# Optimization experiments

Hardware: AMD Instinct MI355X
Metric: run time of the kernel (lower is better)

Reference implementation:

```python
import jax, jax.numpy as jnp
import numpy as np

TEMPERATURE = 8.0
EPS = 1e-8  # torch F.cosine_similarity clamps each norm at eps=1e-8

B, L, H, D = 4, 1024, 8, 64


def setup_inputs() -> dict:
    key = jax.random.key(0)
    kq, kk, kv = jax.random.split(key, 3)
    q = jax.random.normal(kq, (B, L, H, D), dtype=jnp.float32)
    k = jax.random.normal(kk, (B, L, H, D), dtype=jnp.float32)
    v = jax.random.normal(kv, (B, L, H, D), dtype=jnp.float32)
    return {"q": q, "k": k, "v": v}


def _l2_normalize(x):
    # matches torch cosine_similarity: divide by max(||x||, eps)
    n = jnp.sqrt(jnp.sum(x * x, axis=-1, keepdims=True))
    return x / jnp.maximum(n, EPS)


def reference(q, k, v):
    # [B, L, H, D] -> [B, H, L, D]
    qt = jnp.swapaxes(q, 1, 2)
    kt = jnp.swapaxes(k, 1, 2)
    vt = jnpp = jnp.swapaxes(v, 1, 2)
    qn = _l2_normalize(qt)
    kn = _l2_normalize(kt)
    # cosine similarity via matmul instead of O(L*L*D) broadcast
    attn = jnp.einsum("bhid,bhjd->bhij", qn, kn) / TEMPERATURE  # [B,H,L,L]
    attn = jax.nn.softmax(attn, axis=-1)
    out = jnp.einsum("bhij,bhjd->bhid", attn, vt)  # [B,H,L,D]
    return out, attn
```

## Files before the change

### kernel.cpp

```cpp
#include <hip/hip_runtime.h>

#define NB 4
#define NL 1024
#define NH 8
#define ND 64
#define NBH 32

typedef __attribute__((ext_vector_type(8))) short bhalf8;
typedef __attribute__((ext_vector_type(4))) float f32x4;

static __device__ inline unsigned short f2bf(float f) {
    union { float f; unsigned u; } x; x.f = f;
    unsigned r = x.u + 0x7FFFu + ((x.u >> 16) & 1u);
    return (unsigned short)(r >> 16);
}

__global__ __launch_bounds__(256) void norm_qk_kernel(const float* __restrict__ q,
                                                      const float* __restrict__ k,
                                                      unsigned short* __restrict__ qn,
                                                      unsigned short* __restrict__ kn) {
    int wid  = threadIdx.x >> 6;
    int lane = threadIdx.x & 63;
    int r = blockIdx.x * 4 + wid;
    int b = r >> 13;
    int l = (r >> 3) & (NL - 1);
    int h = r & (NH - 1);

    float qv = q[(size_t)r * ND + lane];
    float kv = k[(size_t)r * ND + lane];
    float qs = qv * qv, ks = kv * kv;
    #pragma unroll
    for (int m = 1; m < 64; m <<= 1) {
        qs += __shfl_xor(qs, m);
        ks += __shfl_xor(ks, m);
    }
    float qd = 1.0f / (fmaxf(sqrtf(qs), 1e-8f) * 8.0f);
    float kd = 1.0f / fmaxf(sqrtf(ks), 1e-8f);

    size_t o = ((size_t)(b * NH + h) * NL + l) * ND + lane;
    qn[o] = f2bf(qv * qd);
    kn[o] = f2bf(kv * kd);
}

__global__ __launch_bounds__(256) void vtrans_kernel(const float* __restrict__ v,
                                                     unsigned short* __restrict__ vt) {
    __shared__ float tile[64 * 65];
    int bh = blockIdx.x;
    int b = bh >> 3, h = bh & 7;
    int l0 = blockIdx.y * 64;
    int wid = threadIdx.x >> 6, lane = threadIdx.x & 63;

    #pragma unroll
    for (int rr = 0; rr < 16; ++rr) {
        int row = rr * 4 + wid;
        float val = v[(((size_t)b * NL + l0 + row) * NH + h) * ND + lane];
        tile[lane * 65 + row] = val;
    }
    __syncthreads();
    #pragma unroll
    for (int dd = 0; dd < 16; ++dd) {
        int d = dd * 4 + wid;
        vt[((size_t)(bh * ND + d)) * NL + l0 + lane] = f2bf(tile[d * 65 + lane]);
    }
}

__global__ __launch_bounds__(256) void attn_kernel(const unsigned short* __restrict__ qn,
                                                   const unsigned short* __restrict__ kn,
                                                   const unsigned short* __restrict__ vt,
                                                   float* __restrict__ outp,
                                                   float* __restrict__ attnp) {
    int bh   = blockIdx.x;
    int wid  = threadIdx.x >> 6;
    int lane = threadIdx.x & 63;
    int c    = lane & 15;
    int quad = lane >> 4;
    int qt   = blockIdx.y * 4 + wid;
    int m0   = qt * 16;

    __shared__ __align__(16) unsigned short ptile[4][16 * 40];
    unsigned short* myp = &ptile[wid][0];

    const unsigned short* qbase = qn + ((size_t)(bh * NL + m0 + c)) * ND + quad * 8;
    bhalf8 qa0 = *(const bhalf8*)(qbase);
    bhalf8 qa1 = *(const bhalf8*)(qbase + 32);

    const unsigned short* kbh = kn + (size_t)bh * NL * ND;

    float denom[4] = {0.f, 0.f, 0.f, 0.f};
    for (int jt = 0; jt < 64; ++jt) {
        const unsigned short* kb = kbh + ((size_t)(jt * 16 + c)) * ND + quad * 8;
        bhalf8 kf0 = *(const bhalf8*)(kb);
        bhalf8 kf1 = *(const bhalf8*)(kb + 32);
        f32x4 s = {0.f, 0.f, 0.f, 0.f};
        s = __builtin_amdgcn_mfma_f32_16x16x32_bf16(qa0, kf0, s, 0, 0, 0);
        s = __builtin_amdgcn_mfma_f32_16x16x32_bf16(qa1, kf1, s, 0, 0, 0);
        #pragma unroll
        for (int r = 0; r < 4; ++r) denom[r] += __expf(s[r]);
    }
    #pragma unroll
    for (int r = 0; r < 4; ++r) {
        float d = denom[r];
        d += __shfl_xor(d, 1);
        d += __shfl_xor(d, 2);
        d += __shfl_xor(d, 4);
        d += __shfl_xor(d, 8);
        denom[r] = 1.0f / d;
    }

    float* attnrow = attnp + ((size_t)(bh * NL + m0)) * NL;
    const unsigned short* vbh = vt + (size_t)bh * ND * NL;

    f32x4 o[4] = {{0.f,0.f,0.f,0.f},{0.f,0.f,0.f,0.f},{0.f,0.f,0.f,0.f},{0.f,0.f,0.f,0.f}};
    for (int j2 = 0; j2 < 32; ++j2) {
        int jb = j2 * 32;
        #pragma unroll
        for (int sub = 0; sub < 2; ++sub) {
            int j0 = jb + sub * 16;
            const unsigned short* kb = kbh + ((size_t)(j0 + c)) * ND + quad * 8;
            bhalf8 kf0 = *(const bhalf8*)(kb);
            bhalf8 kf1 = *(const bhalf8*)(kb + 32);
            f32x4 s = {0.f, 0.f, 0.f, 0.f};
            s = __builtin_amdgcn_mfma_f32_16x16x32_bf16(qa0, kf0, s, 0, 0, 0);
            s = __builtin_amdgcn_mfma_f32_16x16x32_bf16(qa1, kf1, s, 0, 0, 0);
            #pragma unroll
            for (int r = 0; r < 4; ++r) {
                float a = __expf(s[r]) * denom[r];
                attnrow[(size_t)(quad * 4 + r) * NL + j0 + c] = a;
                myp[(quad * 4 + r) * 40 + sub * 16 + c] = f2bf(a);
            }
        }
        bhalf8 pa = *(const bhalf8*)(myp + c * 40 + quad * 8);
        #pragma unroll
        for (int nt = 0; nt < 4; ++nt) {
            const unsigned short* vb = vbh + (size_t)(nt * 16 + c) * NL + jb + quad * 8;
            bhalf8 vf = *(const bhalf8*)(vb);
            o[nt] = __builtin_amdgcn_mfma_f32_16x16x32_bf16(pa, vf, o[nt], 0, 0, 0);
        }
    }

    float* obase = outp + ((size_t)(bh * NL + m0)) * ND;
    #pragma unroll
    for (int nt = 0; nt < 4; ++nt) {
        #pragma unroll
        for (int r = 0; r < 4; ++r) {
            obase[(size_t)(quad * 4 + r) * ND + nt * 16 + c] = o[nt][r];
        }
    }
}

extern "C" void kernel_launch(void* const* d_in, const int* in_sizes, int n_in,
                              void* d_out, int out_size, void* d_ws, size_t ws_size,
                              hipStream_t stream) {
    const float* q = (const float*)d_in[0];
    const float* k = (const float*)d_in[1];
    const float* v = (const float*)d_in[2];

    float* outp  = (float*)d_out;
    float* attnp = outp + (size_t)NB * NH * NL * ND;

    unsigned short* qn = (unsigned short*)d_ws;
    unsigned short* kn = qn + (size_t)NB * NH * NL * ND;
    unsigned short* vt = kn + (size_t)NB * NH * NL * ND;

    norm_qk_kernel<<<(NB * NL * NH) / 4, 256, 0, stream>>>(q, k, qn, kn);
    vtrans_kernel<<<dim3(NBH, NL / 64), 256, 0, stream>>>(v, vt);
    attn_kernel<<<dim3(NBH, NL / 16 / 4), 256, 0, stream>>>(qn, kn, vt, outp, attnp);
}
```

Measured before the change: 235.0 us.

## Split key dimension across waves in attention and use exp2 with folded scale

The attention kernel now gives each block one 16-row query tile and splits the 1024 keys across its four waves. Each wave computes a partial softmax denominator and a partial output, and both are combined through shared memory with block barriers. This creates four times as many blocks and shortens each wave's serial key loop. The temperature scaling is folded with log2(e) into the query normalization so the kernel can call the hardware exp2 directly. The V transpose kernel moves to 1024-thread blocks. In exchange, Q fragments are loaded more times and the kernel adds barriers plus a shared-memory reduction.

```diff
diff --git a/kernel.cpp b/kernel.cpp
--- a/kernel.cpp
+++ b/kernel.cpp
@@ -34,7 +34,7 @@
         qs += __shfl_xor(qs, m);
         ks += __shfl_xor(ks, m);
     }
-    float qd = 1.0f / (fmaxf(sqrtf(qs), 1e-8f) * 8.0f);
+    float qd = 1.0f / (fmaxf(sqrtf(qs), 1e-8f) * 5.545177444479562f);
     float kd = 1.0f / fmaxf(sqrtf(ks), 1e-8f);
 
     size_t o = ((size_t)(b * NH + h) * NL + l) * ND + lane;
@@ -42,8 +42,8 @@
     kn[o] = f2bf(kv * kd);
 }
 
-__global__ __launch_bounds__(256) void vtrans_kernel(const float* __restrict__ v,
-                                                     unsigned short* __restrict__ vt) {
+__global__ __launch_bounds__(1024) void vtrans_kernel(const float* __restrict__ v,
+                                                      unsigned short* __restrict__ vt) {
     __shared__ float tile[64 * 65];
     int bh = blockIdx.x;
     int b = bh >> 3, h = bh & 7;
@@ -51,15 +51,15 @@
     int wid = threadIdx.x >> 6, lane = threadIdx.x & 63;
 
     #pragma unroll
-    for (int rr = 0; rr < 16; ++rr) {
-        int row = rr * 4 + wid;
+    for (int rr = 0; rr < 4; ++rr) {
+        int row = wid * 4 + rr;
         float val = v[(((size_t)b * NL + l0 + row) * NH + h) * ND + lane];
         tile[lane * 65 + row] = val;
     }
     __syncthreads();
     #pragma unroll
-    for (int dd = 0; dd < 16; ++dd) {
-        int d = dd * 4 + wid;
+    for (int dd = 0; dd < 4; ++dd) {
+        int d = wid * 4 + dd;
         vt[((size_t)(bh * ND + d)) * NL + l0 + lane] = f2bf(tile[d * 65 + lane]);
     }
 }
@@ -69,16 +69,21 @@
                                                    const unsigned short* __restrict__ vt,
                                                    float* __restrict__ outp,
                                                    float* __restrict__ attnp) {
+    __shared__ __align__(16) unsigned char smem_raw[4 * 16 * 66 * 4];
+    __shared__ float dred[4][16];
+    __shared__ float invd[16];
+
+    unsigned short* ptile = (unsigned short*)smem_raw;
+    float*          oaccf = (float*)smem_raw;
+
     int bh   = blockIdx.x;
     int wid  = threadIdx.x >> 6;
     int lane = threadIdx.x & 63;
     int c    = lane & 15;
     int quad = lane >> 4;
-    int qt   = blockIdx.y * 4 + wid;
-    int m0   = qt * 16;
+    int m0   = blockIdx.y * 16;
 
-    __shared__ __align__(16) unsigned short ptile[4][16 * 40];
-    unsigned short* myp = &ptile[wid][0];
+    unsigned short* myp = ptile + wid * (16 * 40);
 
     const unsigned short* qbase = qn + ((size_t)(bh * NL + m0 + c)) * ND + quad * 8;
     bhalf8 qa0 = *(const bhalf8*)(qbase);
@@ -87,15 +92,16 @@
     const unsigned short* kbh = kn + (size_t)bh * NL * ND;
 
     float denom[4] = {0.f, 0.f, 0.f, 0.f};
-    for (int jt = 0; jt < 64; ++jt) {
-        const unsigned short* kb = kbh + ((size_t)(jt * 16 + c)) * ND + quad * 8;
+    for (int jt = 0; jt < 16; ++jt) {
+        int j0 = wid * 256 + jt * 16;
+        const unsigned short* kb = kbh + ((size_t)(j0 + c)) * ND + quad * 8;
         bhalf8 kf0 = *(const bhalf8*)(kb);
         bhalf8 kf1 = *(const bhalf8*)(kb + 32);
         f32x4 s = {0.f, 0.f, 0.f, 0.f};
         s = __builtin_amdgcn_mfma_f32_16x16x32_bf16(qa0, kf0, s, 0, 0, 0);
         s = __builtin_amdgcn_mfma_f32_16x16x32_bf16(qa1, kf1, s, 0, 0, 0);
         #pragma unroll
-        for (int r = 0; r < 4; ++r) denom[r] += __expf(s[r]);
+        for (int r = 0; r < 4; ++r) denom[r] += __builtin_amdgcn_exp2f(s[r]);
     }
     #pragma unroll
     for (int r = 0; r < 4; ++r) {
@@ -104,15 +110,28 @@
         d += __shfl_xor(d, 2);
         d += __shfl_xor(d, 4);
         d += __shfl_xor(d, 8);
-        denom[r] = 1.0f / d;
+        denom[r] = d;
     }
+    if (c == 0) {
+        #pragma unroll
+        for (int r = 0; r < 4; ++r) dred[wid][quad * 4 + r] = denom[r];
+    }
+    __syncthreads();
+    if (threadIdx.x < 16) {
+        invd[threadIdx.x] = 1.0f / (dred[0][threadIdx.x] + dred[1][threadIdx.x] +
+                                    dred[2][threadIdx.x] + dred[3][threadIdx.x]);
+    }
+    __syncthreads();
+    float inv[4];
+    #pragma unroll
+    for (int r = 0; r < 4; ++r) inv[r] = invd[quad * 4 + r];
 
     float* attnrow = attnp + ((size_t)(bh * NL + m0)) * NL;
     const unsigned short* vbh = vt + (size_t)bh * ND * NL;
 
     f32x4 o[4] = {{0.f,0.f,0.f,0.f},{0.f,0.f,0.f,0.f},{0.f,0.f,0.f,0.f},{0.f,0.f,0.f,0.f}};
-    for (int j2 = 0; j2 < 32; ++j2) {
-        int jb = j2 * 32;
+    for (int j2 = 0; j2 < 8; ++j2) {
+        int jb = wid * 256 + j2 * 32;
         #pragma unroll
         for (int sub = 0; sub < 2; ++sub) {
             int j0 = jb + sub * 16;
@@ -124,7 +143,7 @@
             s = __builtin_amdgcn_mfma_f32_16x16x32_bf16(qa1, kf1, s, 0, 0, 0);
             #pragma unroll
             for (int r = 0; r < 4; ++r) {
-                float a = __expf(s[r]) * denom[r];
+                float a = __builtin_amdgcn_exp2f(s[r]) * inv[r];
                 attnrow[(size_t)(quad * 4 + r) * NL + j0 + c] = a;
                 myp[(quad * 4 + r) * 40 + sub * 16 + c] = f2bf(a);
             }
@@ -138,13 +157,23 @@
         }
     }
 
-    float* obase = outp + ((size_t)(bh * NL + m0)) * ND;
+    __syncthreads();
     #pragma unroll
     for (int nt = 0; nt < 4; ++nt) {
         #pragma unroll
         for (int r = 0; r < 4; ++r) {
-            obase[(size_t)(quad * 4 + r) * ND + nt * 16 + c] = o[nt][r];
+            oaccf[wid * 1056 + (quad * 4 + r) * 66 + nt * 16 + c] = o[nt][r];
         }
+    }
+    __syncthreads();
+    float* obase = outp + ((size_t)(bh * NL + m0)) * ND;
+    #pragma unroll
+    for (int i = 0; i < 4; ++i) {
+        int e = i * 256 + threadIdx.x;
+        int row = e >> 6, col = e & 63;
+        float s = oaccf[row * 66 + col] + oaccf[1056 + row * 66 + col] +
+                  oaccf[2112 + row * 66 + col] + oaccf[3168 + row * 66 + col];
+        obase[e] = s;
     }
 }
 
@@ -163,6 +192,6 @@
     unsigned short* vt = kn + (size_t)NB * NH * NL * ND;
 
     norm_qk_kernel<<<(NB * NL * NH) / 4, 256, 0, stream>>>(q, k, qn, kn);
-    vtrans_kernel<<<dim3(NBH, NL / 64), 256, 0, stream>>>(v, vt);
-    attn_kernel<<<dim3(NBH, NL / 16 / 4), 256, 0, stream>>>(qn, kn, vt, outp, attnp);
+    vtrans_kernel<<<dim3(NBH, NL / 64), 1024, 0, stream>>>(v, vt);
+    attn_kernel<<<dim3(NBH, NL / 16), 256, 0, stream>>>(qn, kn, vt, outp, attnp);
 }
```

New measurement: 236.8 us. Within noise of the previous version (+0.8%).
